# Optimization experiments

Measured on AMD Instinct MI355X. Metric: run time of the kernel, lower is better.

Reference implementation:

```python
import jax, jax.numpy as jnp
import numpy as np

# FFM: 20 fields x 500 features each, k=16
NUM_FIELDS = 20
FIELD_SIZE = 500
TOTAL_FEATURES = NUM_FIELDS * FIELD_SIZE  # 10000
K = 16
BATCH = 4096


def setup_inputs() -> dict:
    key = jax.random.key(0)
    kx, kw, kv = jax.random.split(key, 3)
    x = jax.random.uniform(kx, (BATCH, TOTAL_FEATURES), dtype=jnp.float32)
    w = jax.random.normal(kw, (TOTAL_FEATURES, 1), dtype=jnp.float32)
    v = jax.random.normal(kv, (NUM_FIELDS, TOTAL_FEATURES, K), dtype=jnp.float32)
    return {"x": x, "w": w, "v": v}


def reference(x, w, v):
    B = x.shape[0]
    F, S, k = NUM_FIELDS, FIELD_SIZE, K
    # linear term: [B, 1]
    linear = x @ w
    # group features by field (fields are contiguous, equal-sized)
    xr = x.reshape(B, F, S)            # [b, field i, feat within field]
    vr = v.reshape(F, F, S, k)         # [field g (other), field i, feat, k]
    # E[b, g, i, :] = sum over features of field i of x * v[g]
    # i.e. field-i embedding specialized for interaction with field g
    E = jnp.einsum('bis,gisk->bgik', xr, vr)  # [B, F, F, K]
    # pairwise term: sum_{i<j} <E[b, j, i], E[b, i, j]>
    T = jnp.einsum('bjik,bijk->bij', E, E)    # [B, F, F]
    mask = jnp.triu(jnp.ones((F, F), dtype=bool), 1)
    pair = jnp.sum(jnp.where(mask, T, 0.0), axis=(1, 2))[:, None]  # [B, 1]
    return linear + pair
```

## Files before the change

kernel.cpp:

```cpp
#include <hip/hip_runtime.h>
#include <stdint.h>


#define NF 20
#define FS 500
#define TFEAT 10000
#define KD 16
#define NCOL 336
#define NFRG 21
#define KP 512
#define NB 4096
#define ROWE (NF * NCOL)

typedef __bf16 bf16x8 __attribute__((ext_vector_type(8)));
typedef __bf16 bf16x2 __attribute__((ext_vector_type(2)));
typedef float  f32x4  __attribute__((ext_vector_type(4)));
typedef unsigned int u32x4 __attribute__((ext_vector_type(4)));

typedef __attribute__((address_space(1))) const void* as1cv;
typedef __attribute__((address_space(3))) void* as3v;

__device__ inline void gload_lds16(const void* g, void* l) {
  __builtin_amdgcn_global_load_lds((as1cv)g, (as3v)l, 16, 0, 0);
}

__global__ __launch_bounds__(256) void prep_vt(const float* __restrict__ v,
                                               const float* __restrict__ w,
                                               __bf16* __restrict__ Vt) {
  const int i = blockIdx.x / (NF + 1);
  const int g = blockIdx.x % (NF + 1);
  const int t = threadIdx.x;
  if (g == NF) {
    const float* wf = w + (size_t)i * FS;
    __bf16* o = Vt + ((size_t)i * NCOL + 320) * KP;
    for (int idx = t; idx < 16 * KP; idx += 256) {
      int r = idx >> 9, kk = idx & (KP - 1);
      __bf16 val = (__bf16)0.f;
      if (r == 0 && kk < FS) val = (__bf16)wf[kk];
      o[(size_t)r * KP + kk] = val;
    }
    return;
  }
  __shared__ float lv[FS * 17];
  const int k = t & 15, sb = t >> 4;
  const float* vb = v + ((size_t)g * TFEAT + (size_t)i * FS) * KD;
  for (int it = 0; it < 32; ++it) {
    int s = it * 16 + sb;
    if (s < FS) lv[s * 17 + k] = vb[(size_t)s * KD + k];
  }
  __syncthreads();
  __bf16* out = Vt + ((size_t)i * NCOL + g * 16) * KP;
  for (int r = 0; r < 16; ++r) {
    int s0 = 2 * t, s1 = 2 * t + 1;
    bf16x2 pr;
    pr[0] = (s0 < FS) ? (__bf16)lv[s0 * 17 + r] : (__bf16)0.f;
    pr[1] = (s1 < FS) ? (__bf16)lv[s1 * 17 + r] : (__bf16)0.f;
    *(bf16x2*)(out + (size_t)r * KP + 2 * t) = pr;
  }
}

__global__ __launch_bounds__(256, 3) void k1_gemm(
    const float* __restrict__ x, const __bf16* __restrict__ Vt,
    __bf16* __restrict__ E2, int chunk_base, int tiles) {
  __shared__ __bf16 As[2][64][32];
  __shared__ __bf16 Bs[2][NCOL * 32];

  const int bx = blockIdx.x;
  const int i  = bx / tiles;
  const int tb = bx % tiles;
  const int tid = threadIdx.x;
  const int lane = tid & 63, wid = tid >> 6;
  const int b0 = chunk_base + tb * 64;

  const int arow = tid >> 2;
  const int ac8 = (tid & 3) * 8;
  const int apch = (tid & 3) ^ ((tid >> 3) & 3);
  const float* xrow = x + (size_t)(b0 + arow) * TFEAT + i * FS;
  const int brow_off = lane >> 2;
  const int blc8 = ((lane & 3) ^ ((lane >> 3) & 3)) * 8;
  const __bf16* VtB = Vt + (size_t)i * NCOL * KP;

  f32x4 ar0, ar1;
  auto aload = [&](int t) {
    int kk = t * 32 + ac8;
    int c0 = kk > 496 ? 496 : kk;
    int c1 = kk + 4 > 496 ? 496 : kk + 4;
    ar0 = *(const f32x4*)(xrow + c0);
    ar1 = *(const f32x4*)(xrow + c1);
  };
  auto astore = [&](int buf) {
    bf16x8 h;
    h[0] = (__bf16)ar0[0]; h[1] = (__bf16)ar0[1];
    h[2] = (__bf16)ar0[2]; h[3] = (__bf16)ar0[3];
    h[4] = (__bf16)ar1[0]; h[5] = (__bf16)ar1[1];
    h[6] = (__bf16)ar1[2]; h[7] = (__bf16)ar1[3];
    *(bf16x8*)(&As[buf][arow][apch * 8]) = h;
  };
  auto issueB = [&](int t, int buf) {
    int soffB = t * 32 + blc8;
#pragma unroll
    for (int jj = 0; jj < 6; ++jj) {
      int q = wid + 4 * jj;
      if (q < NFRG)
        gload_lds16(VtB + (size_t)(16 * q + brow_off) * KP + soffB,
                    (void*)&Bs[buf][q * 16 * 32]);
    }
  };

  const int nfr = wid ? 5 : 6;
  const int Fbase = wid ? (1 + wid * 5) : 0;
  const int ar = lane & 15, akc = lane >> 4;

  f32x4 acc[4][6];
#pragma unroll
  for (int m = 0; m < 4; ++m)
#pragma unroll
    for (int nf = 0; nf < 6; ++nf) acc[m][nf] = (f32x4){0.f, 0.f, 0.f, 0.f};

  aload(0);
  issueB(0, 0);
  astore(0);
  asm volatile("s_waitcnt vmcnt(0) lgkmcnt(0)" ::: "memory");
  __builtin_amdgcn_s_barrier();

  for (int t = 0; t < 16; ++t) {
    const int cur = t & 1;
    if (t < 15) {
      aload(t + 1);
      issueB(t + 1, cur ^ 1);
    }
    __builtin_amdgcn_sched_barrier(0);

    bf16x8 bfr[6];
#pragma unroll
    for (int nf = 0; nf < 6; ++nf)
      if (nf < nfr) {
        int n_ = (Fbase + nf) * 16 + ar;
        int pc = akc ^ ((n_ >> 1) & 3);
        bfr[nf] = *(const bf16x8*)&Bs[cur][n_ * 32 + pc * 8];
      }
#pragma unroll
    for (int m = 0; m < 4; ++m) {
      int row = m * 16 + ar;
      int pch = akc ^ ((row >> 1) & 3);
      bf16x8 af = *(const bf16x8*)(&As[cur][row][pch * 8]);
#pragma unroll
      for (int nf = 0; nf < 6; ++nf)
        if (nf < nfr)
          acc[m][nf] = __builtin_amdgcn_mfma_f32_16x16x32_bf16(af, bfr[nf],
                                                               acc[m][nf], 0, 0, 0);
    }
    if (t < 15) {
      astore(cur ^ 1);
      asm volatile("s_waitcnt vmcnt(0) lgkmcnt(0)" ::: "memory");
      __builtin_amdgcn_s_barrier();
    }
  }

  const int lr4 = (lane >> 4) * 4, lcol = lane & 15;
#pragma unroll
  for (int m = 0; m < 4; ++m)
#pragma unroll
    for (int nf = 0; nf < 6; ++nf)
      if (nf < nfr) {
        int n = (Fbase + nf) * 16 + lcol;
#pragma unroll
        for (int r = 0; r < 4; ++r) {
          int bl = tb * 64 + m * 16 + lr4 + r;
          E2[(size_t)bl * ROWE + i * NCOL + n] = (__bf16)acc[m][nf][r];
        }
      }
}

__global__ __launch_bounds__(256) void k2_pair(
    const __bf16* __restrict__ E2, float* __restrict__ out, int chunk_base) {
  __shared__ __align__(16) unsigned shw[4][3360];
  const int tid = threadIdx.x, lane = tid & 63, wid = tid >> 6;
  const int bl = blockIdx.x * 4 + wid;
  const unsigned* src = (const unsigned*)(E2 + (size_t)bl * ROWE);
  for (int it = 0; it < 14; ++it) {
    int idx = it * 64 + lane;
    if (idx < 840) {
      u32x4 val = *(const u32x4*)(src + (size_t)idx * 4);
      *(u32x4*)&shw[wid][idx * 4] = val;
    }
  }
  __syncthreads();
  const __bf16* sh = (const __bf16*)shw[wid];
  const int k = lane & 15, g = lane >> 4;
  float sum = 0.f;
  for (int i = g; i < NF; i += 4)
    for (int j = i + 1; j < NF; ++j)
      sum += (float)sh[i * NCOL + j * 16 + k] * (float)sh[j * NCOL + i * 16 + k];
  if (lane < NF) sum += (float)sh[lane * NCOL + 320];
#pragma unroll
  for (int off = 32; off; off >>= 1) sum += __shfl_xor(sum, off);
  if (lane == 0) out[chunk_base + bl] = sum;
}

extern "C" void kernel_launch(void* const* d_in, const int* in_sizes, int n_in,
                              void* d_out, int out_size, void* d_ws, size_t ws_size,
                              hipStream_t stream) {
  const float* x = (const float*)d_in[0];
  const float* w = (const float*)d_in[1];
  const float* v = (const float*)d_in[2];
  float* out = (float*)d_out;
  char* ws = (char*)d_ws;

  const size_t vt_bytes = (size_t)NF * NCOL * KP * 2;
  __bf16* Vt = (__bf16*)ws;
  __bf16* E2 = (__bf16*)(ws + vt_bytes);

  size_t eavail = (ws_size > vt_bytes) ? ws_size - vt_bytes : 0;
  int Bc = NB;
  while (Bc > 64 && (size_t)Bc * ROWE * 2 > eavail) Bc >>= 1;

  prep_vt<<<NF * (NF + 1), 256, 0, stream>>>(v, w, Vt);
  for (int cb = 0; cb < NB; cb += Bc) {
    int tiles = Bc / 64;
    k1_gemm<<<NF * tiles, 256, 0, stream>>>(x, Vt, E2, cb, tiles);
    k2_pair<<<Bc / 4, 256, 0, stream>>>(E2, out, cb);
  }
}
```

Before: 86.96 us.

## Compute linear term in fp32 alongside GEMM and enlarge tile to 128 rows

Drops the extra 16-column padded fragment that carried the linear weights through the bf16 MFMA GEMM. The linear term is now computed in fp32 from the staged x values against w held in LDS, reduced across lanes and accumulated with atomicAdd into a workspace buffer that k2 adds to the output. The GEMM block grows to 512 threads and 128 batch rows, with a 2x4 warp grid, so each B tile in LDS is reused across twice as many rows. This cuts MFMA work and E2 traffic, at the cost of a memset, atomics, and higher LDS and register pressure per block.

```diff
diff --git a/kernel.cpp b/kernel.cpp
--- a/kernel.cpp
+++ b/kernel.cpp
@@ -6,11 +6,10 @@
 #define FS 500
 #define TFEAT 10000
 #define KD 16
-#define NCOL 336
-#define NFRG 21
+#define NC 320
 #define KP 512
 #define NB 4096
-#define ROWE (NF * NCOL)
+#define ROWE (NF * NC)
 
 typedef __bf16 bf16x8 __attribute__((ext_vector_type(8)));
 typedef __bf16 bf16x2 __attribute__((ext_vector_type(2)));
@@ -25,23 +24,11 @@
 }
 
 __global__ __launch_bounds__(256) void prep_vt(const float* __restrict__ v,
-                                               const float* __restrict__ w,
                                                __bf16* __restrict__ Vt) {
-  const int i = blockIdx.x / (NF + 1);
-  const int g = blockIdx.x % (NF + 1);
+  __shared__ float lv[FS * 17];
+  const int i = blockIdx.x / NF;
+  const int g = blockIdx.x % NF;
   const int t = threadIdx.x;
-  if (g == NF) {
-    const float* wf = w + (size_t)i * FS;
-    __bf16* o = Vt + ((size_t)i * NCOL + 320) * KP;
-    for (int idx = t; idx < 16 * KP; idx += 256) {
-      int r = idx >> 9, kk = idx & (KP - 1);
-      __bf16 val = (__bf16)0.f;
-      if (r == 0 && kk < FS) val = (__bf16)wf[kk];
-      o[(size_t)r * KP + kk] = val;
-    }
-    return;
-  }
-  __shared__ float lv[FS * 17];
   const int k = t & 15, sb = t >> 4;
   const float* vb = v + ((size_t)g * TFEAT + (size_t)i * FS) * KD;
   for (int it = 0; it < 32; ++it) {
@@ -49,7 +36,7 @@
     if (s < FS) lv[s * 17 + k] = vb[(size_t)s * KD + k];
   }
   __syncthreads();
-  __bf16* out = Vt + ((size_t)i * NCOL + g * 16) * KP;
+  __bf16* out = Vt + ((size_t)(i * NC + g * 16)) * KP;
   for (int r = 0; r < 16; ++r) {
     int s0 = 2 * t, s1 = 2 * t + 1;
     bf16x2 pr;
@@ -59,18 +46,21 @@
   }
 }
 
-__global__ __launch_bounds__(256, 3) void k1_gemm(
-    const float* __restrict__ x, const __bf16* __restrict__ Vt,
-    __bf16* __restrict__ E2, int chunk_base, int tiles) {
-  __shared__ __bf16 As[2][64][32];
-  __shared__ __bf16 Bs[2][NCOL * 32];
+__global__ __launch_bounds__(512, 4) void k1_gemm(
+    const float* __restrict__ x, const float* __restrict__ w,
+    const __bf16* __restrict__ Vt, __bf16* __restrict__ E2,
+    float* __restrict__ lin, int chunk_base, int tiles) {
+  __shared__ __bf16 As[2][128][32];
+  __shared__ __bf16 Bs[2][NC * 32];
+  __shared__ float wlds[FS];
 
   const int bx = blockIdx.x;
   const int i  = bx / tiles;
   const int tb = bx % tiles;
   const int tid = threadIdx.x;
   const int lane = tid & 63, wid = tid >> 6;
-  const int b0 = chunk_base + tb * 64;
+  const int wm = wid >> 2, wn = wid & 3;
+  const int b0 = chunk_base + tb * 128;
 
   const int arow = tid >> 2;
   const int ac8 = (tid & 3) * 8;
@@ -78,9 +68,21 @@
   const float* xrow = x + (size_t)(b0 + arow) * TFEAT + i * FS;
   const int brow_off = lane >> 2;
   const int blc8 = ((lane & 3) ^ ((lane >> 3) & 3)) * 8;
-  const __bf16* VtB = Vt + (size_t)i * NCOL * KP;
+  const __bf16* VtB = Vt + (size_t)i * NC * KP;
+
+  auto issueB = [&](int t, int buf) {
+    int soffB = t * 32 + blc8;
+#pragma unroll
+    for (int jj = 0; jj < 3; ++jj) {
+      int q = wid + 8 * jj;
+      if (q < 20)
+        gload_lds16(VtB + (size_t)(16 * q + brow_off) * KP + soffB,
+                    (void*)&Bs[buf][q * 512]);
+    }
+  };
 
   f32x4 ar0, ar1;
+  float lp = 0.f;
   auto aload = [&](int t) {
     int kk = t * 32 + ac8;
     int c0 = kk > 496 ? 496 : kk;
@@ -88,7 +90,18 @@
     ar0 = *(const f32x4*)(xrow + c0);
     ar1 = *(const f32x4*)(xrow + c1);
   };
-  auto astore = [&](int buf) {
+  auto astore = [&](int t, int buf) {
+    int kk = t * 32 + ac8;
+    int c0 = kk > 496 ? 496 : kk;
+    int c1 = kk + 4 > 496 ? 496 : kk + 4;
+    if (kk <= 496) {
+      f32x4 wv = *(const f32x4*)(wlds + c0);
+      lp += ar0[0] * wv[0] + ar0[1] * wv[1] + ar0[2] * wv[2] + ar0[3] * wv[3];
+    }
+    if (kk + 4 <= 496) {
+      f32x4 wv = *(const f32x4*)(wlds + c1);
+      lp += ar1[0] * wv[0] + ar1[1] * wv[1] + ar1[2] * wv[2] + ar1[3] * wv[3];
+    }
     bf16x8 h;
     h[0] = (__bf16)ar0[0]; h[1] = (__bf16)ar0[1];
     h[2] = (__bf16)ar0[2]; h[3] = (__bf16)ar0[3];
@@ -96,30 +109,21 @@
     h[6] = (__bf16)ar1[2]; h[7] = (__bf16)ar1[3];
     *(bf16x8*)(&As[buf][arow][apch * 8]) = h;
   };
-  auto issueB = [&](int t, int buf) {
-    int soffB = t * 32 + blc8;
-#pragma unroll
-    for (int jj = 0; jj < 6; ++jj) {
-      int q = wid + 4 * jj;
-      if (q < NFRG)
-        gload_lds16(VtB + (size_t)(16 * q + brow_off) * KP + soffB,
-                    (void*)&Bs[buf][q * 16 * 32]);
-    }
-  };
-
-  const int nfr = wid ? 5 : 6;
-  const int Fbase = wid ? (1 + wid * 5) : 0;
+
   const int ar = lane & 15, akc = lane >> 4;
 
-  f32x4 acc[4][6];
+  f32x4 acc[4][5];
 #pragma unroll
   for (int m = 0; m < 4; ++m)
 #pragma unroll
-    for (int nf = 0; nf < 6; ++nf) acc[m][nf] = (f32x4){0.f, 0.f, 0.f, 0.f};
-
+    for (int nf = 0; nf < 5; ++nf) acc[m][nf] = (f32x4){0.f, 0.f, 0.f, 0.f};
+
+  for (int c = tid; c < FS; c += 512) wlds[c] = w[i * FS + c];
   aload(0);
   issueB(0, 0);
-  astore(0);
+  asm volatile("s_waitcnt lgkmcnt(0)" ::: "memory");
+  __builtin_amdgcn_s_barrier();
+  astore(0, 0);
   asm volatile("s_waitcnt vmcnt(0) lgkmcnt(0)" ::: "memory");
   __builtin_amdgcn_s_barrier();
 
@@ -131,56 +135,58 @@
     }
     __builtin_amdgcn_sched_barrier(0);
 
-    bf16x8 bfr[6];
-#pragma unroll
-    for (int nf = 0; nf < 6; ++nf)
-      if (nf < nfr) {
-        int n_ = (Fbase + nf) * 16 + ar;
-        int pc = akc ^ ((n_ >> 1) & 3);
-        bfr[nf] = *(const bf16x8*)&Bs[cur][n_ * 32 + pc * 8];
-      }
+    bf16x8 af[4];
 #pragma unroll
     for (int m = 0; m < 4; ++m) {
-      int row = m * 16 + ar;
+      int row = wm * 64 + m * 16 + ar;
       int pch = akc ^ ((row >> 1) & 3);
-      bf16x8 af = *(const bf16x8*)(&As[cur][row][pch * 8]);
-#pragma unroll
-      for (int nf = 0; nf < 6; ++nf)
-        if (nf < nfr)
-          acc[m][nf] = __builtin_amdgcn_mfma_f32_16x16x32_bf16(af, bfr[nf],
-                                                               acc[m][nf], 0, 0, 0);
+      af[m] = *(const bf16x8*)(&As[cur][row][pch * 8]);
+    }
+#pragma unroll
+    for (int nf = 0; nf < 5; ++nf) {
+      int n_ = (wn * 5 + nf) * 16 + ar;
+      int pc = akc ^ ((n_ >> 1) & 3);
+      bf16x8 bfr = *(const bf16x8*)&Bs[cur][n_ * 32 + pc * 8];
+#pragma unroll
+      for (int m = 0; m < 4; ++m)
+        acc[m][nf] = __builtin_amdgcn_mfma_f32_16x16x32_bf16(af[m], bfr,
+                                                             acc[m][nf], 0, 0, 0);
     }
     if (t < 15) {
-      astore(cur ^ 1);
+      astore(t + 1, cur ^ 1);
       asm volatile("s_waitcnt vmcnt(0) lgkmcnt(0)" ::: "memory");
       __builtin_amdgcn_s_barrier();
     }
   }
 
-  const int lr4 = (lane >> 4) * 4, lcol = lane & 15;
+  lp += __shfl_xor(lp, 1);
+  lp += __shfl_xor(lp, 2);
+  if ((tid & 3) == 0) atomicAdd(&lin[b0 + arow], lp);
+
+  const int lr4 = akc * 4;
 #pragma unroll
   for (int m = 0; m < 4; ++m)
 #pragma unroll
-    for (int nf = 0; nf < 6; ++nf)
-      if (nf < nfr) {
-        int n = (Fbase + nf) * 16 + lcol;
-#pragma unroll
-        for (int r = 0; r < 4; ++r) {
-          int bl = tb * 64 + m * 16 + lr4 + r;
-          E2[(size_t)bl * ROWE + i * NCOL + n] = (__bf16)acc[m][nf][r];
-        }
+    for (int nf = 0; nf < 5; ++nf) {
+      int n = (wn * 5 + nf) * 16 + ar;
+#pragma unroll
+      for (int r = 0; r < 4; ++r) {
+        int bl = tb * 128 + wm * 64 + m * 16 + lr4 + r;
+        E2[(size_t)bl * ROWE + i * NC + n] = (__bf16)acc[m][nf][r];
       }
+    }
 }
 
 __global__ __launch_bounds__(256) void k2_pair(
-    const __bf16* __restrict__ E2, float* __restrict__ out, int chunk_base) {
-  __shared__ __align__(16) unsigned shw[4][3360];
+    const __bf16* __restrict__ E2, const float* __restrict__ lin,
+    float* __restrict__ out, int chunk_base) {
+  __shared__ __align__(16) unsigned shw[4][3200];
   const int tid = threadIdx.x, lane = tid & 63, wid = tid >> 6;
   const int bl = blockIdx.x * 4 + wid;
   const unsigned* src = (const unsigned*)(E2 + (size_t)bl * ROWE);
-  for (int it = 0; it < 14; ++it) {
+  for (int it = 0; it < 13; ++it) {
     int idx = it * 64 + lane;
-    if (idx < 840) {
+    if (idx < 800) {
       u32x4 val = *(const u32x4*)(src + (size_t)idx * 4);
       *(u32x4*)&shw[wid][idx * 4] = val;
     }
@@ -191,11 +197,13 @@
   float sum = 0.f;
   for (int i = g; i < NF; i += 4)
     for (int j = i + 1; j < NF; ++j)
-      sum += (float)sh[i * NCOL + j * 16 + k] * (float)sh[j * NCOL + i * 16 + k];
-  if (lane < NF) sum += (float)sh[lane * NCOL + 320];
+      sum += (float)sh[i * NC + j * 16 + k] * (float)sh[j * NC + i * 16 + k];
 #pragma unroll
   for (int off = 32; off; off >>= 1) sum += __shfl_xor(sum, off);
-  if (lane == 0) out[chunk_base + bl] = sum;
+  if (lane == 0) {
+    int bg = chunk_base + bl;
+    out[bg] = lin[bg] + sum;
+  }
 }
 
 extern "C" void kernel_launch(void* const* d_in, const int* in_sizes, int n_in,
@@ -207,18 +215,20 @@
   float* out = (float*)d_out;
   char* ws = (char*)d_ws;
 
-  const size_t vt_bytes = (size_t)NF * NCOL * KP * 2;
+  const size_t vt_bytes = (size_t)NF * NC * KP * 2;
   __bf16* Vt = (__bf16*)ws;
-  __bf16* E2 = (__bf16*)(ws + vt_bytes);
-
-  size_t eavail = (ws_size > vt_bytes) ? ws_size - vt_bytes : 0;
+  float* lin = (float*)(ws + vt_bytes);
+  __bf16* E2 = (__bf16*)(ws + vt_bytes + 16384);
+
+  size_t eavail = (ws_size > vt_bytes + 16384) ? ws_size - vt_bytes - 16384 : 0;
   int Bc = NB;
-  while (Bc > 64 && (size_t)Bc * ROWE * 2 > eavail) Bc >>= 1;
-
-  prep_vt<<<NF * (NF + 1), 256, 0, stream>>>(v, w, Vt);
+  while (Bc > 128 && (size_t)Bc * ROWE * 2 > eavail) Bc >>= 1;
+
+  hipMemsetAsync(lin, 0, NB * sizeof(float), stream);
+  prep_vt<<<NF * NF, 256, 0, stream>>>(v, Vt);
   for (int cb = 0; cb < NB; cb += Bc) {
-    int tiles = Bc / 64;
-    k1_gemm<<<NF * tiles, 256, 0, stream>>>(x, Vt, E2, cb, tiles);
-    k2_pair<<<Bc / 4, 256, 0, stream>>>(E2, out, cb);
-  }
-}
+    int tiles = Bc / 128;
+    k1_gemm<<<NF * tiles, 512, 0, stream>>>(x, w, Vt, E2, lin, cb, tiles);
+    k2_pair<<<Bc / 4, 256, 0, stream>>>(E2, lin, out, cb);
+  }
+}
```

Result: slower. 136.0 us (+56.4%).
